# Kernel optimization log

Hardware: AMD Instinct MI355X
Metric: run time of the kernel (lower is better)

The kernel has to match this reference:

```python
import jax, jax.numpy as jnp
import numpy as np

B, P, H, A = 256, 196, 1024, 512

def setup_inputs() -> dict:
    key = jax.random.key(0)
    ks = jax.random.split(key, 20)
    s = 1.0 / np.sqrt(H)
    sa = 1.0 / np.sqrt(A)
    return {
        "spatial_image": jax.random.normal(ks[0], (B, P, H), jnp.float32),
        "decoder_out": jax.random.normal(ks[1], (B, H), jnp.float32),
        "st": jax.random.normal(ks[2], (B, H), jnp.float32),
        "W_sen_aff": jax.random.uniform(ks[3], (H, H), jnp.float32, -s, s),
        "b_sen_aff": jax.random.uniform(ks[4], (H,), jnp.float32, -s, s),
        "W_sen_att": jax.random.uniform(ks[5], (H, A), jnp.float32, -s, s),
        "b_sen_att": jax.random.uniform(ks[6], (A,), jnp.float32, -s, s),
        "W_h_aff": jax.random.uniform(ks[7], (H, H), jnp.float32, -s, s),
        "b_h_aff": jax.random.uniform(ks[8], (H,), jnp.float32, -s, s),
        "W_h_att": jax.random.uniform(ks[9], (H, A), jnp.float32, -s, s),
        "b_h_att": jax.random.uniform(ks[10], (A,), jnp.float32, -s, s),
        "W_v_att": jax.random.uniform(ks[11], (H, A), jnp.float32, -s, s),
        "b_v_att": jax.random.uniform(ks[12], (A,), jnp.float32, -s, s),
        "W_alpha": jax.random.uniform(ks[13], (A, 1), jnp.float32, -sa, sa),
        "b_alpha": jax.random.uniform(ks[14], (1,), jnp.float32, -sa, sa),
        "W_ctx": jax.random.uniform(ks[15], (H, H), jnp.float32, -s, s),
        "b_ctx": jax.random.uniform(ks[16], (H,), jnp.float32, -s, s),
    }

def reference(spatial_image, decoder_out, st,
              W_sen_aff, b_sen_aff, W_sen_att, b_sen_att,
              W_h_aff, b_h_aff, W_h_att, b_h_att,
              W_v_att, b_v_att, W_alpha, b_alpha, W_ctx, b_ctx):
    # visual_attn: [B, P, A]
    visual_attn = jnp.einsum('bph,ha->bpa', spatial_image, W_v_att) + b_v_att
    # sentinel path: [B, H] -> relu affine -> [B, A]
    sentinel_affine = jax.nn.relu(st @ W_sen_aff + b_sen_aff)
    sentinel_attn = sentinel_affine @ W_sen_att + b_sen_att
    # hidden path: [B, H] -> tanh affine -> [B, A]
    hidden_affine = jnp.tanh(decoder_out @ W_h_aff + b_h_aff)
    hidden_attn = hidden_affine @ W_h_att + b_h_att
    # concat sentinel as an extra "pixel": [B, P+1, H] and [B, P+1, A]
    concat_features = jnp.concatenate([spatial_image, sentinel_affine[:, None, :]], axis=1)
    attended_features = jnp.concatenate([visual_attn, sentinel_attn[:, None, :]], axis=1)
    attention = jnp.tanh(attended_features + hidden_attn[:, None, :])  # [B, P+1, A]
    alpha = (jnp.einsum('bpa,ao->bpo', attention, W_alpha) + b_alpha)[..., 0]  # [B, P+1]
    att_weights = jax.nn.softmax(alpha, axis=1)
    context = jnp.einsum('bph,bp->bh', concat_features, att_weights)  # [B, H]
    beta_value = att_weights[:, -1:]  # [B, 1]
    out_l = jnp.tanh((context + hidden_affine) @ W_ctx + b_ctx)  # [B, H]
    return (out_l, att_weights, beta_value)
```

## Files before the change

### kernel.cpp

```cpp
#include <hip/hip_runtime.h>
#include <hip/hip_bf16.h>
#include <stdint.h>
#include <stddef.h>

typedef __attribute__((ext_vector_type(4))) float f32x4;
typedef __attribute__((ext_vector_type(8))) short short8;

#define MROWS 50176


static __device__ __forceinline__ int lds_off(int row, int k) {
    int slot = (k >> 3) ^ ((row >> 1) & 3);
    return (row << 6) + (slot << 4) + ((k & 7) << 1);
}

static __device__ __forceinline__ unsigned div196(unsigned g) {
    return (unsigned)(((unsigned long long)g * 85599ull) >> 24);
}

static __device__ __forceinline__ unsigned short f2bf(float f) {
    union { float f; unsigned u; } v; v.f = f;
    unsigned r = v.u + 0x7FFFu + ((v.u >> 16) & 1u);
    return (unsigned short)(r >> 16);
}

static __device__ __forceinline__ unsigned long long pack4bf(f32x4 a) {
    union { unsigned long long u; __hip_bfloat162 h[2]; } r;
    r.h[0] = __float22bfloat162_rn(make_float2(a[0], a[1]));
    r.h[1] = __float22bfloat162_rn(make_float2(a[2], a[3]));
    return r.u;
}

static __device__ __forceinline__ float tanh_fast(float x) {
    float xc = fminf(fmaxf(x, -9.f), 9.f);
    float e = __builtin_amdgcn_exp2f(xc * 2.885390081777927f);
    return (e - 1.f) * __builtin_amdgcn_rcpf(e + 1.f);
}

static __device__ __forceinline__ void gload_lds16(const void* g, void* l) {
    __builtin_amdgcn_global_load_lds(
        (const __attribute__((address_space(1))) unsigned int*)g,
        (__attribute__((address_space(3))) unsigned int*)l, 16, 0, 0);
}

static __device__ __forceinline__ void kloop_dbuf(
    const float* __restrict__ Abase,
    const unsigned short* __restrict__ Bbase,
    char* sA0, char* sA1, char* sB0, char* sB1,
    f32x4 acc[4][4], int tid)
{
    const int lane = tid & 63, w = tid >> 6;
    const int lrow = lane & 15, lk = lane >> 4;
    const int wr = w >> 1, wc = w & 1;

    const float* Ap[4];
    int aoff[4];
    #pragma unroll
    for (int r = 0; r < 4; ++r) {
        int q = tid + (r << 8);
        int ar = q >> 3, kc = (q & 7) << 2;
        Ap[r] = Abase + (size_t)ar * 1024 + kc;
        aoff[r] = lds_off(ar, kc);
    }
    const unsigned short* Bp[2];
    int bdst[2];
    #pragma unroll
    for (int c = 0; c < 2; ++c) {
        int ch = (w << 1) + c;
        int row = (ch << 4) + (lane >> 2);
        int kg = (lane & 3) ^ ((row >> 1) & 3);
        Bp[c] = Bbase + (size_t)row * 1024 + (kg << 3);
        bdst[c] = ch << 10;
    }

    f32x4 z = {0.f, 0.f, 0.f, 0.f};
    #pragma unroll
    for (int m = 0; m < 4; ++m)
        #pragma unroll
        for (int n = 0; n < 4; ++n) acc[m][n] = z;

    {
        f32x4 a[4];
        #pragma unroll
        for (int r = 0; r < 4; ++r) a[r] = *(const f32x4*)Ap[r];
        #pragma unroll
        for (int c = 0; c < 2; ++c) gload_lds16(Bp[c], sB0 + bdst[c]);
        #pragma unroll
        for (int r = 0; r < 4; ++r)
            *(unsigned long long*)(sA0 + aoff[r]) = pack4bf(a[r]);
    }
    __syncthreads();

    char* sAc = sA0; char* sAn = sA1;
    char* sBc = sB0; char* sBn = sB1;
    for (int ks = 0; ks < 32; ++ks) {
        f32x4 an[4];
        if (ks < 31) {
            const int ko = (ks + 1) << 5;
            #pragma unroll
            for (int r = 0; r < 4; ++r) an[r] = *(const f32x4*)(Ap[r] + ko);
            #pragma unroll
            for (int c = 0; c < 2; ++c) gload_lds16(Bp[c] + ko, sBn + bdst[c]);
        }
        short8 af[4], bf[4];
        #pragma unroll
        for (int m = 0; m < 4; ++m)
            af[m] = *(const short8*)(sAc + lds_off((wr << 6) + (m << 4) + lrow, lk << 3));
        #pragma unroll
        for (int n = 0; n < 4; ++n)
            bf[n] = *(const short8*)(sBc + lds_off((wc << 6) + (n << 4) + lrow, lk << 3));
        #pragma unroll
        for (int m = 0; m < 4; ++m)
            #pragma unroll
            for (int n = 0; n < 4; ++n)
                acc[m][n] = __builtin_amdgcn_mfma_f32_16x16x32_bf16(af[m], bf[n], acc[m][n], 0, 0, 0);
        if (ks < 31) {
            #pragma unroll
            for (int r = 0; r < 4; ++r)
                *(unsigned long long*)(sAn + aoff[r]) = pack4bf(an[r]);
        }
        __syncthreads();
        char* t;
        t = sAc; sAc = sAn; sAn = t;
        t = sBc; sBc = sBn; sBn = t;
    }
}

__global__ __launch_bounds__(256, 4) void attn_alpha_kernel(
    const float* __restrict__ spatial,
    const unsigned short* __restrict__ WvT,
    const float* __restrict__ b_v_att,
    const float* __restrict__ hidden_attn,
    const float* __restrict__ W_alpha,
    float* __restrict__ alphap)
{
    __shared__ char sA[2][8192];
    __shared__ char sB[2][8192];
    __shared__ float alpha_s[2][128];
    const int tid = threadIdx.x;
    const int j = blockIdx.x;
    const int wk = (j & 7) * 196 + (j >> 3);
    const int mt = wk >> 2, n4 = wk & 3;
    const int row0 = mt << 7, col0 = n4 << 7;

    f32x4 acc[4][4];
    kloop_dbuf(spatial + (size_t)row0 * 1024, WvT + (size_t)col0 * 1024,
               sA[0], sA[1], sB[0], sB[1], acc, tid);

    const int lane = tid & 63, w = tid >> 6;
    const int wr = w >> 1, wc = w & 1;
    const int lrow = lane & 15, lk = lane >> 4;

    const unsigned bb0 = div196((unsigned)row0);
    const unsigned bb1 = div196((unsigned)(row0 + 127));
    float bv[4], wa[4], h0[4], h1[4];
    #pragma unroll
    for (int n = 0; n < 4; ++n) {
        int g = col0 + (wc << 6) + (n << 4) + lrow;
        bv[n] = b_v_att[g];
        wa[n] = W_alpha[g];
        h0[n] = hidden_attn[bb0 * 512 + g];
        h1[n] = hidden_attn[bb1 * 512 + g];
    }
    #pragma unroll
    for (int m = 0; m < 4; ++m) {
        #pragma unroll
        for (int i = 0; i < 4; ++i) {
            int rloc = (wr << 6) + (m << 4) + (lk << 2) + i;
            bool first = (div196((unsigned)(row0 + rloc)) == bb0);
            float s = 0.f;
            #pragma unroll
            for (int n = 0; n < 4; ++n) {
                float v = tanh_fast(acc[m][n][i] + bv[n] + (first ? h0[n] : h1[n]));
                s += v * wa[n];
            }
            #pragma unroll
            for (int off = 1; off < 16; off <<= 1) s += __shfl_xor(s, off);
            if (lrow == 0) alpha_s[wc][rloc] = s;
        }
    }
    __syncthreads();
    if (tid < 128)
        alphap[(size_t)n4 * MROWS + row0 + tid] = alpha_s[0][tid] + alpha_s[1][tid];
}

struct GemmDesc { const float* A; const unsigned short* BT; const float* bias; float* C; int N; int act; };
struct GemmPair { GemmDesc d[2]; };

__global__ __launch_bounds__(256, 4) void gemm_pair_kernel(GemmPair p)
{
    GemmDesc d = p.d[blockIdx.z];
    __shared__ char sA[2][8192];
    __shared__ char sB[2][8192];
    const int tid = threadIdx.x;
    const int row0 = blockIdx.x << 7;
    const int col0 = blockIdx.y << 7;
    f32x4 acc[4][4];
    kloop_dbuf(d.A + (size_t)row0 * 1024, d.BT + (size_t)col0 * 1024,
               sA[0], sA[1], sB[0], sB[1], acc, tid);
    const int lane = tid & 63, w = tid >> 6;
    const int wr = w >> 1, wc = w & 1;
    const int lrow = lane & 15, lk = lane >> 4;
    #pragma unroll
    for (int n = 0; n < 4; ++n) {
        int col = col0 + (wc << 6) + (n << 4) + lrow;
        float bs = d.bias[col];
        #pragma unroll
        for (int m = 0; m < 4; ++m) {
            int rbase = row0 + (wr << 6) + (m << 4) + (lk << 2);
            #pragma unroll
            for (int i = 0; i < 4; ++i) {
                float v = acc[m][n][i] + bs;
                if (d.act == 1) v = fmaxf(v, 0.f);
                if (d.act == 2) v = tanh_fast(v);
                d.C[(size_t)(rbase + i) * d.N + col] = v;
            }
        }
    }
}

struct TransDesc { const float* src; unsigned short* dst; int K; int N; };
struct TransArgs { TransDesc d[6]; };

__global__ void transpose_cvt_kernel(TransArgs args) {
    TransDesc d = args.d[blockIdx.y];
    int nt = d.N >> 5;
    int tiles = (d.K >> 5) * nt;
    if ((int)blockIdx.x >= tiles) return;
    int tk = blockIdx.x / nt, tn = blockIdx.x % nt;
    __shared__ unsigned short tile[32][33];
    int tx = threadIdx.x & 31, ty = threadIdx.x >> 5;
    int k0 = tk << 5, n0 = tn << 5;
    #pragma unroll
    for (int j = 0; j < 4; ++j)
        tile[ty + j * 8][tx] = f2bf(d.src[(size_t)(k0 + ty + j * 8) * d.N + n0 + tx]);
    __syncthreads();
    #pragma unroll
    for (int j = 0; j < 4; ++j)
        d.dst[(size_t)(n0 + ty + j * 8) * d.K + k0 + tx] = tile[tx][ty + j * 8];
}

__global__ void softmax_sentinel_kernel(
    const float* __restrict__ alphap,
    const float* __restrict__ sen_att, const float* __restrict__ hid_att,
    const float* __restrict__ W_alpha,
    float* __restrict__ att, float* __restrict__ beta)
{
    int b = blockIdx.x, tid = threadIdx.x;
    __shared__ float al[197];
    __shared__ float red[4];
    if (tid < 196) {
        size_t g = (size_t)b * 196 + tid;
        al[tid] = alphap[g] + alphap[MROWS + g] + alphap[2 * MROWS + g] + alphap[3 * MROWS + g];
    }
    float s = 0.f;
    for (int a = tid; a < 512; a += 256)
        s += tanh_fast(sen_att[b * 512 + a] + hid_att[b * 512 + a]) * W_alpha[a];
    #pragma unroll
    for (int off = 1; off < 64; off <<= 1) s += __shfl_xor(s, off);
    if ((tid & 63) == 0) red[tid >> 6] = s;
    __syncthreads();
    if (tid == 0) al[196] = red[0] + red[1] + red[2] + red[3];
    __syncthreads();
    if (tid < 64) {
        float v[4];
        float mx = -1e30f;
        #pragma unroll
        for (int jj = 0; jj < 4; ++jj) {
            int i = tid + jj * 64;
            v[jj] = (i < 197) ? al[i] : -1e30f;
            mx = fmaxf(mx, v[jj]);
        }
        #pragma unroll
        for (int off = 1; off < 64; off <<= 1) mx = fmaxf(mx, __shfl_xor(mx, off));
        float sm = 0.f;
        #pragma unroll
        for (int jj = 0; jj < 4; ++jj) {
            v[jj] = __builtin_amdgcn_exp2f((v[jj] - mx) * 1.442695040888963f);
            if (tid + jj * 64 >= 197) v[jj] = 0.f;
            sm += v[jj];
        }
        #pragma unroll
        for (int off = 1; off < 64; off <<= 1) sm += __shfl_xor(sm, off);
        float inv = 1.f / sm;
        #pragma unroll
        for (int jj = 0; jj < 4; ++jj) {
            int i = tid + jj * 64;
            if (i < 197) {
                float wv = v[jj] * inv;
                att[b * 197 + i] = wv;
                if (i == 196) beta[b] = wv;
            }
        }
    }
}

__global__ __launch_bounds__(256) void context_kernel(
    const float* __restrict__ spatial, const float* __restrict__ sen_aff,
    const float* __restrict__ hid_aff, const float* __restrict__ att,
    float* __restrict__ ctxh)
{
    int b = blockIdx.x, half = blockIdx.y, t = threadIdx.x;
    __shared__ float wsm[197];
    if (t < 197) wsm[t] = att[b * 197 + t];
    __syncthreads();
    int h2 = (half << 8) + t;
    const float2* sp = (const float2*)(spatial + (size_t)b * 196 * 1024) + h2;
    float ax = 0.f, ay = 0.f;
    #pragma unroll 8
    for (int p = 0; p < 196; ++p) {
        float2 x = sp[(size_t)p * 512];
        ax += wsm[p] * x.x; ay += wsm[p] * x.y;
    }
    float w196 = wsm[196];
    float2 sa = ((const float2*)(sen_aff + (size_t)b * 1024))[h2];
    float2 ha = ((const float2*)(hid_aff + (size_t)b * 1024))[h2];
    ctxh[(size_t)b * 1024 + 2 * h2]     = ax + w196 * sa.x + ha.x;
    ctxh[(size_t)b * 1024 + 2 * h2 + 1] = ay + w196 * sa.y + ha.y;
}

extern "C" void kernel_launch(void* const* d_in, const int* in_sizes, int n_in,
                              void* d_out, int out_size, void* d_ws, size_t ws_size,
                              hipStream_t stream)
{
    const float* spatial   = (const float*)d_in[0];
    const float* decoder   = (const float*)d_in[1];
    const float* st        = (const float*)d_in[2];
    const float* W_sen_aff = (const float*)d_in[3];
    const float* b_sen_aff = (const float*)d_in[4];
    const float* W_sen_att = (const float*)d_in[5];
    const float* b_sen_att = (const float*)d_in[6];
    const float* W_h_aff   = (const float*)d_in[7];
    const float* b_h_aff   = (const float*)d_in[8];
    const float* W_h_att   = (const float*)d_in[9];
    const float* b_h_att   = (const float*)d_in[10];
    const float* W_v_att   = (const float*)d_in[11];
    const float* b_v_att   = (const float*)d_in[12];
    const float* W_alpha   = (const float*)d_in[13];
    const float* W_ctx     = (const float*)d_in[15];
    const float* b_ctx     = (const float*)d_in[16];

    char* ws = (char*)d_ws;
    size_t off = 0;
    auto alloc = [&](size_t bytes) {
        char* p = ws + off; off += (bytes + 255) & ~(size_t)255; return p;
    };
    unsigned short* WvT  = (unsigned short*)alloc((size_t)512 * 1024 * 2);
    unsigned short* WsaT = (unsigned short*)alloc((size_t)1024 * 1024 * 2);
    unsigned short* WstT = (unsigned short*)alloc((size_t)512 * 1024 * 2);
    unsigned short* WhaT = (unsigned short*)alloc((size_t)1024 * 1024 * 2);
    unsigned short* WhtT = (unsigned short*)alloc((size_t)512 * 1024 * 2);
    unsigned short* WcxT = (unsigned short*)alloc((size_t)1024 * 1024 * 2);
    float* sen_aff = (float*)alloc((size_t)256 * 1024 * 4);
    float* sen_att = (float*)alloc((size_t)256 * 512 * 4);
    float* hid_aff = (float*)alloc((size_t)256 * 1024 * 4);
    float* hid_att = (float*)alloc((size_t)256 * 512 * 4);
    float* alphap  = (float*)alloc((size_t)4 * MROWS * 4);
    float* ctxh    = (float*)alloc((size_t)256 * 1024 * 4);

    float* out_l    = (float*)d_out;
    float* out_att  = out_l + 256 * 1024;
    float* out_beta = out_att + 256 * 197;

    TransArgs ta;
    ta.d[0] = { W_v_att,   WvT,  1024, 512  };
    ta.d[1] = { W_sen_aff, WsaT, 1024, 1024 };
    ta.d[2] = { W_sen_att, WstT, 1024, 512  };
    ta.d[3] = { W_h_aff,   WhaT, 1024, 1024 };
    ta.d[4] = { W_h_att,   WhtT, 1024, 512  };
    ta.d[5] = { W_ctx,     WcxT, 1024, 1024 };
    transpose_cvt_kernel<<<dim3(1024, 6), 256, 0, stream>>>(ta);

    GemmPair p1;
    p1.d[0] = { st,      WsaT, b_sen_aff, sen_aff, 1024, 1 };
    p1.d[1] = { decoder, WhaT, b_h_aff,   hid_aff, 1024, 2 };
    gemm_pair_kernel<<<dim3(2, 8, 2), 256, 0, stream>>>(p1);

    GemmPair p2;
    p2.d[0] = { sen_aff, WstT, b_sen_att, sen_att, 512, 0 };
    p2.d[1] = { hid_aff, WhtT, b_h_att,   hid_att, 512, 0 };
    gemm_pair_kernel<<<dim3(2, 4, 2), 256, 0, stream>>>(p2);

    attn_alpha_kernel<<<1568, 256, 0, stream>>>(spatial, WvT, b_v_att, hid_att, W_alpha, alphap);
    softmax_sentinel_kernel<<<256, 256, 0, stream>>>(alphap, sen_att, hid_att, W_alpha, out_att, out_beta);
    context_kernel<<<dim3(256, 2), 256, 0, stream>>>(spatial, sen_aff, hid_aff, out_att, ctxh);

    GemmPair p3;
    p3.d[0] = { ctxh, WcxT, b_ctx, out_l, 1024, 2 };
    p3.d[1] = { ctxh, WcxT, b_ctx, out_l, 1024, 2 };
    gemm_pair_kernel<<<dim3(2, 8, 1), 256, 0, stream>>>(p3);
}
```

Measured before the change: 217.1 us.

## Deepen attention GEMM pipeline with triple-buffered B and two-ahead prefetch

Replaces the double-buffered K loop in the attention-alpha GEMM with a deeper pipeline. B tiles get three LDS buffers and are fetched two steps ahead by direct global-to-LDS loads. A tiles are held in registers two steps ahead, and the MFMA block runs at raised wave priority. Explicit vmcnt/lgkmcnt waits plus a raw barrier replace __syncthreads, so memory latency can overlap more compute. The cost is extra LDS and registers, with launch bounds lowered from 4 to 3 blocks per CU, which reduces occupancy.

New measurement: 224.6 us (median of 2 runs). 1.03x slower.

```diff
diff --git a/kernel.cpp b/kernel.cpp
--- a/kernel.cpp
+++ b/kernel.cpp
@@ -43,11 +43,53 @@
         (__attribute__((address_space(3))) unsigned int*)l, 16, 0, 0);
 }
 
-static __device__ __forceinline__ void kloop_dbuf(
+template<bool PREF, bool LATE, int VEND>
+static __device__ __forceinline__ void pipe_step(
+    int t,
+    const float* const (&Ap)[4], const int (&aoff)[4],
+    const unsigned short* const (&Bp)[2], const int (&bdst)[2],
+    char* sAcur, char* sAnxt, char* sB, int bc, int bn,
+    f32x4 (&aCon)[4], f32x4 (&aFill)[4], f32x4 (&acc)[4][4],
+    int wr, int wc, int lrow, int lk)
+{
+    char* sBc = sB + (bc << 13);
+    if (PREF) {
+        char* sBn = sB + (bn << 13);
+        const int ko = (t + 2) << 5;
+        gload_lds16(Bp[0] + ko, sBn + bdst[0]);
+        gload_lds16(Bp[1] + ko, sBn + bdst[1]);
+        #pragma unroll
+        for (int r = 0; r < 4; ++r) aFill[r] = *(const f32x4*)(Ap[r] + ko);
+    }
+    short8 af[4], bf[4];
+    #pragma unroll
+    for (int m = 0; m < 4; ++m)
+        af[m] = *(const short8*)(sAcur + lds_off((wr << 6) + (m << 4) + lrow, lk << 3));
+    #pragma unroll
+    for (int n = 0; n < 4; ++n)
+        bf[n] = *(const short8*)(sBc + lds_off((wc << 6) + (n << 4) + lrow, lk << 3));
+    __builtin_amdgcn_s_setprio(1);
+    #pragma unroll
+    for (int m = 0; m < 4; ++m)
+        #pragma unroll
+        for (int n = 0; n < 4; ++n)
+            acc[m][n] = __builtin_amdgcn_mfma_f32_16x16x32_bf16(af[m], bf[n], acc[m][n], 0, 0, 0);
+    __builtin_amdgcn_s_setprio(0);
+    if (LATE) {
+        #pragma unroll
+        for (int r = 0; r < 4; ++r)
+            *(unsigned long long*)(sAnxt + aoff[r]) = pack4bf(aCon[r]);
+        asm volatile("s_waitcnt vmcnt(%0)" :: "n"(VEND) : "memory");
+        asm volatile("s_waitcnt lgkmcnt(0)" ::: "memory");
+        __builtin_amdgcn_s_barrier();
+    }
+}
+
+static __device__ __forceinline__ void kloop_pipe(
     const float* __restrict__ Abase,
     const unsigned short* __restrict__ Bbase,
-    char* sA0, char* sA1, char* sB0, char* sB1,
-    f32x4 acc[4][4], int tid)
+    char* sA, char* sB,
+    f32x4 (&acc)[4][4], int tid)
 {
     const int lane = tid & 63, w = tid >> 6;
     const int lrow = lane & 15, lk = lane >> 4;
@@ -79,6 +121,134 @@
         #pragma unroll
         for (int n = 0; n < 4; ++n) acc[m][n] = z;
 
+    f32x4 aX[4], aY[4];
+
+    gload_lds16(Bp[0], sB + bdst[0]);
+    gload_lds16(Bp[1], sB + bdst[1]);
+    gload_lds16(Bp[0] + 32, sB + 8192 + bdst[0]);
+    gload_lds16(Bp[1] + 32, sB + 8192 + bdst[1]);
+    #pragma unroll
+    for (int r = 0; r < 4; ++r) aX[r] = *(const f32x4*)Ap[r];
+    asm volatile("s_waitcnt vmcnt(0)" ::: "memory");
+    #pragma unroll
+    for (int r = 0; r < 4; ++r)
+        *(unsigned long long*)(sA + aoff[r]) = pack4bf(aX[r]);
+    #pragma unroll
+    for (int r = 0; r < 4; ++r) aY[r] = *(const f32x4*)(Ap[r] + 32);
+    asm volatile("s_waitcnt lgkmcnt(0)" ::: "memory");
+    __builtin_amdgcn_s_barrier();
+
+    int bc = 0, bn = 2;
+    #pragma unroll 1
+    for (int t = 0; t < 30; t += 2) {
+        pipe_step<true, true, 6>(t, Ap, aoff, Bp, bdst,
+            sA, sA + 8192, sB, bc, bn, aY, aX, acc, wr, wc, lrow, lk);
+        bc = (bc == 2) ? 0 : bc + 1;  bn = (bn == 2) ? 0 : bn + 1;
+        pipe_step<true, true, 6>(t + 1, Ap, aoff, Bp, bdst,
+            sA + 8192, sA, sB, bc, bn, aX, aY, acc, wr, wc, lrow, lk);
+        bc = (bc == 2) ? 0 : bc + 1;  bn = (bn == 2) ? 0 : bn + 1;
+    }
+    pipe_step<false, true, 0>(30, Ap, aoff, Bp, bdst,
+        sA, sA + 8192, sB, bc, bn, aY, aX, acc, wr, wc, lrow, lk);
+    bc = (bc == 2) ? 0 : bc + 1;
+    pipe_step<false, false, 0>(31, Ap, aoff, Bp, bdst,
+        sA + 8192, sA, sB, bc, bn, aX, aY, acc, wr, wc, lrow, lk);
+}
+
+__global__ __launch_bounds__(256, 3) void attn_alpha_kernel(
+    const float* __restrict__ spatial,
+    const unsigned short* __restrict__ WvT,
+    const float* __restrict__ b_v_att,
+    const float* __restrict__ hidden_attn,
+    const float* __restrict__ W_alpha,
+    float* __restrict__ alphap)
+{
+    __shared__ char sA[2][8192];
+    __shared__ char sB[3][8192];
+    __shared__ float alpha_s[2][128];
+    const int tid = threadIdx.x;
+    const int j = blockIdx.x;
+    const int wk = (j & 7) * 196 + (j >> 3);
+    const int mt = wk >> 2, n4 = wk & 3;
+    const int row0 = mt << 7, col0 = n4 << 7;
+
+    f32x4 acc[4][4];
+    kloop_pipe(spatial + (size_t)row0 * 1024, WvT + (size_t)col0 * 1024,
+               &sA[0][0], &sB[0][0], acc, tid);
+
+    const int lane = tid & 63, w = tid >> 6;
+    const int wr = w >> 1, wc = w & 1;
+    const int lrow = lane & 15, lk = lane >> 4;
+
+    const unsigned bb0 = div196((unsigned)row0);
+    const unsigned bb1 = div196((unsigned)(row0 + 127));
+    float bv[4], wa[4], h0[4], h1[4];
+    #pragma unroll
+    for (int n = 0; n < 4; ++n) {
+        int g = col0 + (wc << 6) + (n << 4) + lrow;
+        bv[n] = b_v_att[g];
+        wa[n] = W_alpha[g];
+        h0[n] = hidden_attn[bb0 * 512 + g];
+        h1[n] = hidden_attn[bb1 * 512 + g];
+    }
+    #pragma unroll
+    for (int m = 0; m < 4; ++m) {
+        #pragma unroll
+        for (int i = 0; i < 4; ++i) {
+            int rloc = (wr << 6) + (m << 4) + (lk << 2) + i;
+            bool first = (div196((unsigned)(row0 + rloc)) == bb0);
+            float s = 0.f;
+            #pragma unroll
+            for (int n = 0; n < 4; ++n) {
+                float v = tanh_fast(acc[m][n][i] + bv[n] + (first ? h0[n] : h1[n]));
+                s += v * wa[n];
+            }
+            #pragma unroll
+            for (int off = 1; off < 16; off <<= 1) s += __shfl_xor(s, off);
+            if (lrow == 0) alpha_s[wc][rloc] = s;
+        }
+    }
+    __syncthreads();
+    if (tid < 128)
+        alphap[(size_t)n4 * MROWS + row0 + tid] = alpha_s[0][tid] + alpha_s[1][tid];
+}
+
+static __device__ __forceinline__ void kloop_dbuf(
+    const float* __restrict__ Abase,
+    const unsigned short* __restrict__ Bbase,
+    char* sA0, char* sA1, char* sB0, char* sB1,
+    f32x4 acc[4][4], int tid)
+{
+    const int lane = tid & 63, w = tid >> 6;
+    const int lrow = lane & 15, lk = lane >> 4;
+    const int wr = w >> 1, wc = w & 1;
+
+    const float* Ap[4];
+    int aoff[4];
+    #pragma unroll
+    for (int r = 0; r < 4; ++r) {
+        int q = tid + (r << 8);
+        int ar = q >> 3, kc = (q & 7) << 2;
+        Ap[r] = Abase + (size_t)ar * 1024 + kc;
+        aoff[r] = lds_off(ar, kc);
+    }
+    const unsigned short* Bp[2];
+    int bdst[2];
+    #pragma unroll
+    for (int c = 0; c < 2; ++c) {
+        int ch = (w << 1) + c;
+        int row = (ch << 4) + (lane >> 2);
+        int kg = (lane & 3) ^ ((row >> 1) & 3);
+        Bp[c] = Bbase + (size_t)row * 1024 + (kg << 3);
+        bdst[c] = ch << 10;
+    }
+
+    f32x4 z = {0.f, 0.f, 0.f, 0.f};
+    #pragma unroll
+    for (int m = 0; m < 4; ++m)
+        #pragma unroll
+        for (int n = 0; n < 4; ++n) acc[m][n] = z;
+
     {
         f32x4 a[4];
         #pragma unroll
@@ -124,64 +294,6 @@
         t = sAc; sAc = sAn; sAn = t;
         t = sBc; sBc = sBn; sBn = t;
     }
-}
-
-__global__ __launch_bounds__(256, 4) void attn_alpha_kernel(
-    const float* __restrict__ spatial,
-    const unsigned short* __restrict__ WvT,
-    const float* __restrict__ b_v_att,
-    const float* __restrict__ hidden_attn,
-    const float* __restrict__ W_alpha,
-    float* __restrict__ alphap)
-{
-    __shared__ char sA[2][8192];
-    __shared__ char sB[2][8192];
-    __shared__ float alpha_s[2][128];
-    const int tid = threadIdx.x;
-    const int j = blockIdx.x;
-    const int wk = (j & 7) * 196 + (j >> 3);
-    const int mt = wk >> 2, n4 = wk & 3;
-    const int row0 = mt << 7, col0 = n4 << 7;
-
-    f32x4 acc[4][4];
-    kloop_dbuf(spatial + (size_t)row0 * 1024, WvT + (size_t)col0 * 1024,
-               sA[0], sA[1], sB[0], sB[1], acc, tid);
-
-    const int lane = tid & 63, w = tid >> 6;
-    const int wr = w >> 1, wc = w & 1;
-    const int lrow = lane & 15, lk = lane >> 4;
-
-    const unsigned bb0 = div196((unsigned)row0);
-    const unsigned bb1 = div196((unsigned)(row0 + 127));
-    float bv[4], wa[4], h0[4], h1[4];
-    #pragma unroll
-    for (int n = 0; n < 4; ++n) {
-        int g = col0 + (wc << 6) + (n << 4) + lrow;
-        bv[n] = b_v_att[g];
-        wa[n] = W_alpha[g];
-        h0[n] = hidden_attn[bb0 * 512 + g];
-        h1[n] = hidden_attn[bb1 * 512 + g];
-    }
-    #pragma unroll
-    for (int m = 0; m < 4; ++m) {
-        #pragma unroll
-        for (int i = 0; i < 4; ++i) {
-            int rloc = (wr << 6) + (m << 4) + (lk << 2) + i;
-            bool first = (div196((unsigned)(row0 + rloc)) == bb0);
-            float s = 0.f;
-            #pragma unroll
-            for (int n = 0; n < 4; ++n) {
-                float v = tanh_fast(acc[m][n][i] + bv[n] + (first ? h0[n] : h1[n]));
-                s += v * wa[n];
-            }
-            #pragma unroll
-            for (int off = 1; off < 16; off <<= 1) s += __shfl_xor(s, off);
-            if (lrow == 0) alpha_s[wc][rloc] = s;
-        }
-    }
-    __syncthreads();
-    if (tid < 128)
-        alphap[(size_t)n4 * MROWS + row0 + tid] = alpha_s[0][tid] + alpha_s[1][tid];
 }
 
 struct GemmDesc { const float* A; const unsigned short* BT; const float* bias; float* C; int N; int act; };
```

## Widen attention-alpha GEMM tile to full 512 columns per block

Applied to the files above, without the earlier changes.

The visual-attention GEMM now uses 512-thread blocks that each compute a 128x512 tile covering the whole attention dimension. Each spatial row is therefore read and converted to bf16 once instead of four times. The alpha reduction is finished in shared memory with atomics, which removes the four partial alpha buffers and the summation in the softmax kernel. In exchange there are fewer blocks (392 instead of 1568), 64KB of LDS for B per block, more accumulator registers, and MFMA priority hints, all of which put occupancy and latency hiding at risk.

Result: slower. 240.5 us (+10.8%).

```diff
diff --git a/kernel.cpp b/kernel.cpp
--- a/kernel.cpp
+++ b/kernel.cpp
@@ -41,6 +41,128 @@
     __builtin_amdgcn_global_load_lds(
         (const __attribute__((address_space(1))) unsigned int*)g,
         (__attribute__((address_space(3))) unsigned int*)l, 16, 0, 0);
+}
+
+__global__ __launch_bounds__(512, 2) void attn_alpha_kernel(
+    const float* __restrict__ spatial,
+    const unsigned short* __restrict__ WvT,
+    const float* __restrict__ b_v_att,
+    const float* __restrict__ hidden_attn,
+    const float* __restrict__ W_alpha,
+    float* __restrict__ alphab)
+{
+    __shared__ char sA[2][8192];
+    __shared__ char sB[2][32768];
+    float* alpha_s = (float*)&sA[0][0];
+    const int tid = threadIdx.x;
+    const int row0 = blockIdx.x << 7;
+
+    const int lane = tid & 63, w = tid >> 6;
+    const int wr = w >> 2, wc = w & 3;
+    const int lrow = lane & 15, lk = lane >> 4;
+
+    const int arow = tid >> 3;
+    const int acol = (tid & 7) << 2;
+    const float* Ap = spatial + (size_t)(row0 + arow) * 1024 + acol;
+    const int aoff0 = lds_off(arow, acol);
+    const int aoff1 = lds_off(arow + 64, acol);
+
+    const int kg = (lane & 3) ^ ((lane >> 3) & 3);
+    const unsigned short* Bp = WvT + (size_t)((w << 4) + (lane >> 2)) * 1024 + (kg << 3);
+
+    f32x4 acc[4][8];
+    f32x4 z = {0.f, 0.f, 0.f, 0.f};
+    #pragma unroll
+    for (int m = 0; m < 4; ++m)
+        #pragma unroll
+        for (int n = 0; n < 8; ++n) acc[m][n] = z;
+
+    {
+        f32x4 a0 = *(const f32x4*)(Ap);
+        f32x4 a1 = *(const f32x4*)(Ap + 64 * 1024);
+        #pragma unroll
+        for (int r = 0; r < 4; ++r)
+            gload_lds16(Bp + ((size_t)r << 17), sB[0] + (r << 13) + (w << 10));
+        *(unsigned long long*)(sA[0] + aoff0) = pack4bf(a0);
+        *(unsigned long long*)(sA[0] + aoff1) = pack4bf(a1);
+    }
+    __syncthreads();
+
+    int cur = 0;
+    #pragma unroll 1
+    for (int ks = 0; ks < 32; ++ks) {
+        const int nxt = cur ^ 1;
+        f32x4 a0n, a1n;
+        if (ks < 31) {
+            const float* Apk = Ap + ((ks + 1) << 5);
+            a0n = *(const f32x4*)(Apk);
+            a1n = *(const f32x4*)(Apk + 64 * 1024);
+            const unsigned short* Bpk = Bp + ((ks + 1) << 5);
+            #pragma unroll
+            for (int r = 0; r < 4; ++r)
+                gload_lds16(Bpk + ((size_t)r << 17), sB[nxt] + (r << 13) + (w << 10));
+        }
+        short8 af[4], bf[8];
+        #pragma unroll
+        for (int m = 0; m < 4; ++m)
+            af[m] = *(const short8*)(sA[cur] + lds_off((wr << 6) + (m << 4) + lrow, lk << 3));
+        #pragma unroll
+        for (int n = 0; n < 8; ++n)
+            bf[n] = *(const short8*)(sB[cur] + lds_off((wc << 7) + (n << 4) + lrow, lk << 3));
+        __builtin_amdgcn_s_setprio(1);
+        #pragma unroll
+        for (int m = 0; m < 4; ++m)
+            #pragma unroll
+            for (int n = 0; n < 8; ++n)
+                acc[m][n] = __builtin_amdgcn_mfma_f32_16x16x32_bf16(af[m], bf[n], acc[m][n], 0, 0, 0);
+        __builtin_amdgcn_s_setprio(0);
+        if (ks < 31) {
+            *(unsigned long long*)(sA[nxt] + aoff0) = pack4bf(a0n);
+            *(unsigned long long*)(sA[nxt] + aoff1) = pack4bf(a1n);
+        }
+        __syncthreads();
+        cur = nxt;
+    }
+
+    if (tid < 128) alpha_s[tid] = 0.f;
+    __syncthreads();
+
+    const unsigned bb0 = div196((unsigned)row0);
+    const unsigned bb1 = div196((unsigned)(row0 + 127));
+    float bv[8], wa[8], h0[8], h1[8];
+    #pragma unroll
+    for (int n = 0; n < 8; ++n) {
+        int g = (wc << 7) + (n << 4) + lrow;
+        bv[n] = b_v_att[g];
+        wa[n] = W_alpha[g];
+        h0[n] = hidden_attn[bb0 * 512 + g];
+        h1[n] = hidden_attn[bb1 * 512 + g];
+    }
+    #pragma unroll
+    for (int m = 0; m < 4; ++m) {
+        int rloc0 = (wr << 6) + (m << 4) + (lk << 2);
+        #pragma unroll
+        for (int i = 0; i < 4; ++i) {
+            unsigned g = (unsigned)(row0 + rloc0 + i);
+            bool first = (div196(g) == bb0);
+            float s = 0.f;
+            #pragma unroll
+            for (int n = 0; n < 8; ++n) {
+                float v = tanh_fast(acc[m][n][i] + bv[n] + (first ? h0[n] : h1[n]));
+                s += v * wa[n];
+            }
+            #pragma unroll
+            for (int off = 1; off < 16; off <<= 1) s += __shfl_xor(s, off);
+            if (lrow == 0) atomicAdd(&alpha_s[rloc0 + i], s);
+        }
+    }
+    __syncthreads();
+    if (tid < 128) {
+        unsigned g = (unsigned)(row0 + tid);
+        unsigned bb = div196(g);
+        unsigned p = g - bb * 196;
+        alphab[bb * 196 + p] = alpha_s[tid];
+    }
 }
 
 static __device__ __forceinline__ void kloop_dbuf(
@@ -124,64 +246,6 @@
         t = sAc; sAc = sAn; sAn = t;
         t = sBc; sBc = sBn; sBn = t;
     }
-}
-
-__global__ __launch_bounds__(256, 4) void attn_alpha_kernel(
-    const float* __restrict__ spatial,
-    const unsigned short* __restrict__ WvT,
-    const float* __restrict__ b_v_att,
-    const float* __restrict__ hidden_attn,
-    const float* __restrict__ W_alpha,
-    float* __restrict__ alphap)
-{
-    __shared__ char sA[2][8192];
-    __shared__ char sB[2][8192];
-    __shared__ float alpha_s[2][128];
-    const int tid = threadIdx.x;
-    const int j = blockIdx.x;
-    const int wk = (j & 7) * 196 + (j >> 3);
-    const int mt = wk >> 2, n4 = wk & 3;
-    const int row0 = mt << 7, col0 = n4 << 7;
-
-    f32x4 acc[4][4];
-    kloop_dbuf(spatial + (size_t)row0 * 1024, WvT + (size_t)col0 * 1024,
-               sA[0], sA[1], sB[0], sB[1], acc, tid);
-
-    const int lane = tid & 63, w = tid >> 6;
-    const int wr = w >> 1, wc = w & 1;
-    const int lrow = lane & 15, lk = lane >> 4;
-
-    const unsigned bb0 = div196((unsigned)row0);
-    const unsigned bb1 = div196((unsigned)(row0 + 127));
-    float bv[4], wa[4], h0[4], h1[4];
-    #pragma unroll
-    for (int n = 0; n < 4; ++n) {
-        int g = col0 + (wc << 6) + (n << 4) + lrow;
-        bv[n] = b_v_att[g];
-        wa[n] = W_alpha[g];
-        h0[n] = hidden_attn[bb0 * 512 + g];
-        h1[n] = hidden_attn[bb1 * 512 + g];
-    }
-    #pragma unroll
-    for (int m = 0; m < 4; ++m) {
-        #pragma unroll
-        for (int i = 0; i < 4; ++i) {
-            int rloc = (wr << 6) + (m << 4) + (lk << 2) + i;
-            bool first = (div196((unsigned)(row0 + rloc)) == bb0);
-            float s = 0.f;
-            #pragma unroll
-            for (int n = 0; n < 4; ++n) {
-                float v = tanh_fast(acc[m][n][i] + bv[n] + (first ? h0[n] : h1[n]));
-                s += v * wa[n];
-            }
-            #pragma unroll
-            for (int off = 1; off < 16; off <<= 1) s += __shfl_xor(s, off);
-            if (lrow == 0) alpha_s[wc][rloc] = s;
-        }
-    }
-    __syncthreads();
-    if (tid < 128)
-        alphap[(size_t)n4 * MROWS + row0 + tid] = alpha_s[0][tid] + alpha_s[1][tid];
 }
 
 struct GemmDesc { const float* A; const unsigned short* BT; const float* bias; float* C; int N; int act; };
@@ -241,7 +305,7 @@
 }
 
 __global__ void softmax_sentinel_kernel(
-    const float* __restrict__ alphap,
+    const float* __restrict__ alphab,
     const float* __restrict__ sen_att, const float* __restrict__ hid_att,
     const float* __restrict__ W_alpha,
     float* __restrict__ att, float* __restrict__ beta)
@@ -249,10 +313,7 @@
     int b = blockIdx.x, tid = threadIdx.x;
     __shared__ float al[197];
     __shared__ float red[4];
-    if (tid < 196) {
-        size_t g = (size_t)b * 196 + tid;
-        al[tid] = alphap[g] + alphap[MROWS + g] + alphap[2 * MROWS + g] + alphap[3 * MROWS + g];
-    }
+    if (tid < 196) al[tid] = alphab[b * 196 + tid];
     float s = 0.f;
     for (int a = tid; a < 512; a += 256)
         s += tanh_fast(sen_att[b * 512 + a] + hid_att[b * 512 + a]) * W_alpha[a];
@@ -355,7 +416,7 @@
     float* sen_att = (float*)alloc((size_t)256 * 512 * 4);
     float* hid_aff = (float*)alloc((size_t)256 * 1024 * 4);
     float* hid_att = (float*)alloc((size_t)256 * 512 * 4);
-    float* alphap  = (float*)alloc((size_t)4 * MROWS * 4);
+    float* alphab  = (float*)alloc((size_t)MROWS * 4);
     float* ctxh    = (float*)alloc((size_t)256 * 1024 * 4);
 
     float* out_l    = (float*)d_out;
@@ -381,8 +442,8 @@
     p2.d[1] = { hid_aff, WhtT, b_h_att,   hid_att, 512, 0 };
     gemm_pair_kernel<<<dim3(2, 4, 2), 256, 0, stream>>>(p2);
 
-    attn_alpha_kernel<<<1568, 256, 0, stream>>>(spatial, WvT, b_v_att, hid_att, W_alpha, alphap);
-    softmax_sentinel_kernel<<<256, 256, 0, stream>>>(alphap, sen_att, hid_att, W_alpha, out_att, out_beta);
+    attn_alpha_kernel<<<392, 512, 0, stream>>>(spatial, WvT, b_v_att, hid_att, W_alpha, alphab);
+    softmax_sentinel_kernel<<<256, 256, 0, stream>>>(alphab, sen_att, hid_att, W_alpha, out_att, out_beta);
     context_kernel<<<dim3(256, 2), 256, 0, stream>>>(spatial, sen_aff, hid_aff, out_att, ctxh);
 
     GemmPair p3;
```
